# Optimization experiments

Measured on AMD Instinct MI355X. Metric: run time of the kernel, lower is better.

## Reference

```python
import jax, jax.numpy as jnp
import numpy as np

B, T, C, H = 4, 2048, 768, 12
D = C // H  # head dim = 64

def setup_inputs() -> dict:
    key = jax.random.key(0)
    k1, k2, k3, k4, k5 = jax.random.split(key, 5)
    s = 0.02
    x = jax.random.normal(k1, (B, T, C), dtype=jnp.float32)
    w_qkv = jax.random.normal(k2, (3 * C, C), dtype=jnp.float32) * s  # torch Linear weight [out,in]
    b_qkv = jax.random.normal(k3, (3 * C,), dtype=jnp.float32) * s
    w_proj = jax.random.normal(k4, (C, C), dtype=jnp.float32) * s
    b_proj = jax.random.normal(k5, (C,), dtype=jnp.float32) * s
    return {"x": x, "w_qkv": w_qkv, "b_qkv": b_qkv, "w_proj": w_proj, "b_proj": b_proj}

def reference(x, w_qkv, b_qkv, w_proj, b_proj):
    Bx, Tx, Cx = x.shape
    # qkv projection: torch Linear y = x @ W.T + b
    qkv = x @ w_qkv.T + b_qkv                      # [B,T,3C]
    qkv = qkv.reshape(Bx, Tx, 3, H, D)
    q, k, v = qkv[:, :, 0], qkv[:, :, 1], qkv[:, :, 2]  # each [B,T,H,D]
    scale = 1.0 / jnp.sqrt(jnp.float32(D))
    scores = jnp.einsum('bqhd,bkhd->bhqk', q, k) * scale  # [B,H,T,T]
    causal = jnp.tril(jnp.ones((Tx, Tx), dtype=bool))
    scores = jnp.where(causal[None, None], scores, -jnp.inf)
    attn = jax.nn.softmax(scores, axis=-1)
    out = jnp.einsum('bhqk,bkhd->bqhd', attn, v).reshape(Bx, Tx, Cx)
    return out @ w_proj.T + b_proj
```

## Files before the change

kernel.cpp:

```cpp
#include <hip/hip_runtime.h>
#include <hip/hip_bf16.h>
#include <cstdint>
#include <cstddef>

typedef __bf16 bf16_t;
typedef __bf16 bf16x8 __attribute__((ext_vector_type(8)));
typedef __bf16 bf16x4 __attribute__((ext_vector_type(4)));
typedef float f32x4 __attribute__((ext_vector_type(4)));
typedef float f32x16 __attribute__((ext_vector_type(16)));

constexpr int B_ = 4, T_ = 2048, C_ = 768, H_ = 12, D_ = 64;
constexpr size_t QKV_ELEMS = (size_t)B_ * H_ * T_ * D_;

__device__ __forceinline__ void gload16(const bf16_t* g, bf16_t* l) {
    __builtin_amdgcn_global_load_lds(
        (const __attribute__((address_space(1))) unsigned int*)g,
        (__attribute__((address_space(3))) unsigned int*)l, 16, 0, 0);
}

__global__ __launch_bounds__(256)
void conv_bf16(const float* __restrict__ a, bf16_t* __restrict__ oa, int na8,
               const float* __restrict__ b, bf16_t* __restrict__ ob, int nb8)
{
    int i = blockIdx.x * 256 + threadIdx.x;
    if (i >= na8 + nb8) return;
    const float* src; bf16_t* dst; int idx;
    if (i < na8) { src = a; dst = oa; idx = i; }
    else         { src = b; dst = ob; idx = i - na8; }
    const float4* p = reinterpret_cast<const float4*>(src + (size_t)idx * 8);
    float4 f0 = p[0], f1 = p[1];
    bf16x8 t;
    t[0]=(bf16_t)f0.x; t[1]=(bf16_t)f0.y; t[2]=(bf16_t)f0.z; t[3]=(bf16_t)f0.w;
    t[4]=(bf16_t)f1.x; t[5]=(bf16_t)f1.y; t[6]=(bf16_t)f1.z; t[7]=(bf16_t)f1.w;
    *reinterpret_cast<bf16x8*>(dst + (size_t)idx * 8) = t;
}

__global__ __launch_bounds__(256, 3)
void qkv_gemm(const bf16_t* __restrict__ xb, const bf16_t* __restrict__ wb,
              const float* __restrict__ bias,
              bf16_t* __restrict__ q, bf16_t* __restrict__ k, bf16_t* __restrict__ v)
{
    __shared__ alignas(16) bf16_t As[128 * 64];
    __shared__ alignas(16) bf16_t Bs[128 * 64];
    const int tid  = threadIdx.x;
    const int lane = tid & 63;
    const int w    = tid >> 6;
    const int wm = w >> 1, wn = w & 1;
    const int bm = blockIdx.x & 63;
    const int bn = blockIdx.x >> 6;
    const int m0 = bm * 128, n0 = bn * 128;
    const int lcol = lane & 15, lgrp = lane >> 4;
    const int srow = lane >> 3;
    const int scol = ((lane & 7) ^ srow) * 8;

    const bf16_t* ag = xb + (size_t)(m0 + w * 32 + srow) * C_ + scol;
    const bf16_t* bg = wb + (size_t)(n0 + w * 32 + srow) * C_ + scol;
    bf16_t* al = &As[(w * 32) * 64];
    bf16_t* bl = &Bs[(w * 32) * 64];

    f32x4 acc[4][4] = {};

    for (int kt = 0; kt < C_; kt += 64) {
        __syncthreads();
        #pragma unroll
        for (int p = 0; p < 4; ++p) {
            gload16(ag + (size_t)(p * 8) * C_ + kt, al + p * 8 * 64);
            gload16(bg + (size_t)(p * 8) * C_ + kt, bl + p * 8 * 64);
        }
        __syncthreads();
        #pragma unroll
        for (int kk = 0; kk < 2; ++kk) {
            bf16x8 af[4], bfr[4];
            #pragma unroll
            for (int i = 0; i < 4; ++i) {
                const int R = wm * 64 + i * 16 + lcol;
                af[i] = *reinterpret_cast<const bf16x8*>(&As[R * 64 + (((kk*4 + lgrp) ^ (R & 7)) << 3)]);
            }
            #pragma unroll
            for (int j = 0; j < 4; ++j) {
                const int R = wn * 64 + j * 16 + lcol;
                bfr[j] = *reinterpret_cast<const bf16x8*>(&Bs[R * 64 + (((kk*4 + lgrp) ^ (R & 7)) << 3)]);
            }
            #pragma unroll
            for (int i = 0; i < 4; ++i)
                #pragma unroll
                for (int j = 0; j < 4; ++j)
                    acc[i][j] = __builtin_amdgcn_mfma_f32_16x16x32_bf16(af[i], bfr[j], acc[i][j], 0, 0, 0);
        }
    }

    #pragma unroll
    for (int j = 0; j < 4; ++j) {
        const int n = n0 + wn * 64 + j * 16 + lcol;
        const float bv = bias[n];
        const int s = n / C_, rem = n % C_;
        const int h = rem >> 6, d = rem & 63;
        bf16_t* dst = (s == 0) ? q : (s == 1) ? k : v;
        #pragma unroll
        for (int i = 0; i < 4; ++i) {
            #pragma unroll
            for (int r = 0; r < 4; ++r) {
                const int m = m0 + wm * 64 + i * 16 + lgrp * 4 + r;
                const int b = m >> 11, t = m & (T_ - 1);
                dst[(((size_t)(b * H_ + h)) * T_ + t) * D_ + d] = (bf16_t)(acc[i][j][r] + bv);
            }
        }
    }
}

__global__ __launch_bounds__(128, 3)
void attn_fwd(const bf16_t* __restrict__ qg, const bf16_t* __restrict__ kg,
              const bf16_t* __restrict__ vg, bf16_t* __restrict__ og)
{
    __shared__ alignas(16) bf16_t Ks[64 * 64];
    __shared__ alignas(16) bf16_t Vt[64 * 64];

    const int tid  = threadIdx.x;
    const int lane = tid & 63;
    const int w    = tid >> 6;
    const int l31  = lane & 31;
    const int hi   = lane >> 5;
    const int qi   = blockIdx.x / 48;
    const int bh   = blockIdx.x % 48;
    const int qt   = 31 - qi;
    const int q0   = qt * 64;
    const int qw   = q0 + w * 32;
    const size_t base = (size_t)bh * T_ * D_;
    const int qrow = qw + l31;

    const float SCL = 0.125f * 1.44269504f;
    bf16x8 bq[4];
    #pragma unroll
    for (int kt = 0; kt < 4; ++kt) {
        bf16x8 t = *reinterpret_cast<const bf16x8*>(qg + base + (size_t)qrow * D_ + kt*16 + hi*8);
        #pragma unroll
        for (int e = 0; e < 8; ++e) t[e] = (bf16_t)((float)t[e] * SCL);
        bq[kt] = t;
    }

    f32x16 ot0 = {};
    f32x16 ot1 = {};
    float m = -1e30f, rowl = 0.0f;

    const int skey = tid >> 3;
    const int sgr  = tid & 7;
    const bf16_t* srcK = kg + base + (size_t)skey * D_ + sgr * 8;
    const bf16_t* srcV = vg + base + (size_t)(2 * skey) * D_ + sgr * 8;

    union U8 { bf16x8 v; uint32_t u[4]; };
    U8 kr[4], vr[2][2];

    #pragma unroll
    for (int p = 0; p < 4; ++p)
        kr[p].v = *reinterpret_cast<const bf16x8*>(srcK + (size_t)(p * 16) * D_);
    #pragma unroll
    for (int p = 0; p < 2; ++p) {
        vr[p][0].v = *reinterpret_cast<const bf16x8*>(srcV + (size_t)(p * 32) * D_);
        vr[p][1].v = *reinterpret_cast<const bf16x8*>(srcV + (size_t)(p * 32 + 1) * D_);
    }

    union UP { uint32_t u[4]; bf16x8 v; };

    const int ntiles = qt + 1;
    for (int it = 0; it < ntiles; ++it) {
        __syncthreads();
        #pragma unroll
        for (int p = 0; p < 4; ++p) {
            const int key = p * 16 + skey;
            *reinterpret_cast<bf16x8*>(Ks + key * 64 + ((sgr ^ (key & 7)) << 3)) = kr[p].v;
        }
        #pragma unroll
        for (int p = 0; p < 2; ++p) {
            const int va = p * 16 + skey;
            #pragma unroll
            for (int j = 0; j < 8; ++j) {
                const int d = sgr * 8 + j;
                const int ss = ((va >> 2) ^ j ^ sgr) & 7;
                uint32_t wd = __builtin_amdgcn_perm(vr[p][1].u[j >> 1], vr[p][0].u[j >> 1],
                                                    (j & 1) ? 0x07060302u : 0x05040100u);
                *reinterpret_cast<uint32_t*>(Vt + d * 64 + ss * 8 + (va & 3) * 2) = wd;
            }
        }
        __syncthreads();
        if (it + 1 < ntiles) {
            const size_t soff = (size_t)(it + 1) * 64 * D_;
            #pragma unroll
            for (int p = 0; p < 4; ++p)
                kr[p].v = *reinterpret_cast<const bf16x8*>(srcK + soff + (size_t)(p * 16) * D_);
            #pragma unroll
            for (int p = 0; p < 2; ++p) {
                vr[p][0].v = *reinterpret_cast<const bf16x8*>(srcV + soff + (size_t)(p * 32) * D_);
                vr[p][1].v = *reinterpret_cast<const bf16x8*>(srcV + soff + (size_t)(p * 32 + 1) * D_);
            }
        }

        const int kv0 = it * 64;
        #pragma unroll
        for (int sk = 0; sk < 2; ++sk) {
            const int kvs = kv0 + sk * 32;
            if (sk == 1 && kvs > qw + 31) continue;

            f32x16 s = {};
            __builtin_amdgcn_s_setprio(1);
            #pragma unroll
            for (int kt = 0; kt < 4; ++kt) {
                const int keyl = sk * 32 + l31;
                const int slot = kt * 2 + hi;
                bf16x8 ka = *reinterpret_cast<const bf16x8*>(
                    Ks + keyl * 64 + ((slot ^ (keyl & 7)) << 3));
                s = __builtin_amdgcn_mfma_f32_32x32x16_bf16(ka, bq[kt], s, 0, 0, 0);
            }
            __builtin_amdgcn_s_setprio(0);
            if (kvs + 31 > qw) {
                #pragma unroll
                for (int r = 0; r < 16; ++r) {
                    const int key = kvs + (r & 3) + 8 * (r >> 2) + 4 * hi;
                    if (key > qrow) s[r] = -1e30f;
                }
            }
            float a0 = fmaxf(fmaxf(s[0],  s[1]),  s[2]);
            float a1 = fmaxf(fmaxf(s[3],  s[4]),  s[5]);
            float a2 = fmaxf(fmaxf(s[6],  s[7]),  s[8]);
            float a3 = fmaxf(fmaxf(s[9],  s[10]), s[11]);
            float a4 = fmaxf(fmaxf(s[12], s[13]), s[14]);
            float b0 = fmaxf(fmaxf(a0, a1), a2);
            float b1 = fmaxf(fmaxf(a3, a4), s[15]);
            float mt = fmaxf(b0, b1);
            mt = fmaxf(mt, __shfl_xor(mt, 32));
            if (!__all(mt <= m + 8.0f)) {
                const float mnew = fmaxf(m, mt);
                const float alpha = exp2f(m - mnew);
                #pragma unroll
                for (int r = 0; r < 16; ++r) { ot0[r] *= alpha; ot1[r] *= alpha; }
                rowl *= alpha;
                m = mnew;
            }
            #pragma unroll
            for (int r = 0; r < 16; ++r) s[r] = exp2f(s[r] - m);
            float t0 = (s[0]+s[1]) + (s[2]+s[3]);
            float t1 = (s[4]+s[5]) + (s[6]+s[7]);
            float t2 = (s[8]+s[9]) + (s[10]+s[11]);
            float t3 = (s[12]+s[13]) + (s[14]+s[15]);
            float rs = (t0 + t1) + (t2 + t3);
            rs += __shfl_xor(rs, 32);
            rowl += rs;

            uint32_t c0, c1, c2, c3, c4, c5, c6, c7;
            asm("v_cvt_pk_bf16_f32 %0, %1, %2" : "=v"(c0) : "v"(s[0]),  "v"(s[1]));
            asm("v_cvt_pk_bf16_f32 %0, %1, %2" : "=v"(c1) : "v"(s[2]),  "v"(s[3]));
            asm("v_cvt_pk_bf16_f32 %0, %1, %2" : "=v"(c2) : "v"(s[4]),  "v"(s[5]));
            asm("v_cvt_pk_bf16_f32 %0, %1, %2" : "=v"(c3) : "v"(s[6]),  "v"(s[7]));
            asm("v_cvt_pk_bf16_f32 %0, %1, %2" : "=v"(c4) : "v"(s[8]),  "v"(s[9]));
            asm("v_cvt_pk_bf16_f32 %0, %1, %2" : "=v"(c5) : "v"(s[10]), "v"(s[11]));
            asm("v_cvt_pk_bf16_f32 %0, %1, %2" : "=v"(c6) : "v"(s[12]), "v"(s[13]));
            asm("v_cvt_pk_bf16_f32 %0, %1, %2" : "=v"(c7) : "v"(s[14]), "v"(s[15]));
            asm("v_permlane32_swap_b32 %0, %1" : "+v"(c0), "+v"(c2));
            asm("v_permlane32_swap_b32 %0, %1" : "+v"(c1), "+v"(c3));
            asm("v_permlane32_swap_b32 %0, %1" : "+v"(c4), "+v"(c6));
            asm("v_permlane32_swap_b32 %0, %1" : "+v"(c5), "+v"(c7));
            UP pa0; pa0.u[0] = c0; pa0.u[1] = c1; pa0.u[2] = c2; pa0.u[3] = c3;
            UP pa1; pa1.u[0] = c4; pa1.u[1] = c5; pa1.u[2] = c6; pa1.u[3] = c7;

            __builtin_amdgcn_s_setprio(1);
            #pragma unroll
            for (int dblk = 0; dblk < 2; ++dblk) {
                const int d = dblk * 32 + l31;
                f32x16& o = dblk ? ot1 : ot0;
                #pragma unroll
                for (int ktile = 0; ktile < 2; ++ktile) {
                    const int kslot = sk * 4 + ktile * 2 + hi;
                    const int ss = kslot ^ (d & 7) ^ ((d >> 3) & 7);
                    bf16x8 va = *reinterpret_cast<const bf16x8*>(Vt + d * 64 + (ss << 3));
                    o = __builtin_amdgcn_mfma_f32_32x32x16_bf16(va, ktile ? pa1.v : pa0.v, o, 0, 0, 0);
                }
            }
            __builtin_amdgcn_s_setprio(0);
        }
    }

    const int b = bh / H_, h = bh % H_;
    const float inv = 1.0f / rowl;
    bf16_t* dst = &og[((size_t)b * T_ + qrow) * C_ + h * D_];
    #pragma unroll
    for (int dblk = 0; dblk < 2; ++dblk) {
        const f32x16& o = dblk ? ot1 : ot0;
        #pragma unroll
        for (int qd = 0; qd < 4; ++qd) {
            bf16x4 v4;
            #pragma unroll
            for (int r = 0; r < 4; ++r) v4[r] = (bf16_t)(o[qd * 4 + r] * inv);
            *reinterpret_cast<bf16x4*>(dst + dblk * 32 + qd * 8 + hi * 4) = v4;
        }
    }
}

__global__ __launch_bounds__(256, 3)
void proj_gemm(const bf16_t* __restrict__ ao, const bf16_t* __restrict__ wpb,
               const float* __restrict__ bias, float* __restrict__ out)
{
    __shared__ alignas(16) bf16_t As[128 * 64];
    __shared__ alignas(16) bf16_t Bs[128 * 64];
    const int tid  = threadIdx.x;
    const int lane = tid & 63;
    const int w    = tid >> 6;
    const int wm = w >> 1, wn = w & 1;
    const int bm = blockIdx.x & 63;
    const int bn = blockIdx.x >> 6;
    const int m0 = bm * 128, n0 = bn * 128;
    const int lcol = lane & 15, lgrp = lane >> 4;
    const int srow = lane >> 3;
    const int scol = ((lane & 7) ^ srow) * 8;

    const bf16_t* ag = ao  + (size_t)(m0 + w * 32 + srow) * C_ + scol;
    const bf16_t* bg = wpb + (size_t)(n0 + w * 32 + srow) * C_ + scol;
    bf16_t* al = &As[(w * 32) * 64];
    bf16_t* bl = &Bs[(w * 32) * 64];

    f32x4 acc[4][4] = {};

    for (int kt = 0; kt < C_; kt += 64) {
        __syncthreads();
        #pragma unroll
        for (int p = 0; p < 4; ++p) {
            gload16(ag + (size_t)(p * 8) * C_ + kt, al + p * 8 * 64);
            gload16(bg + (size_t)(p * 8) * C_ + kt, bl + p * 8 * 64);
        }
        __syncthreads();
        #pragma unroll
        for (int kk = 0; kk < 2; ++kk) {
            bf16x8 af[4], bfr[4];
            #pragma unroll
            for (int i = 0; i < 4; ++i) {
                const int R = wm * 64 + i * 16 + lcol;
                af[i] = *reinterpret_cast<const bf16x8*>(&As[R * 64 + (((kk*4 + lgrp) ^ (R & 7)) << 3)]);
            }
            #pragma unroll
            for (int j = 0; j < 4; ++j) {
                const int R = wn * 64 + j * 16 + lcol;
                bfr[j] = *reinterpret_cast<const bf16x8*>(&Bs[R * 64 + (((kk*4 + lgrp) ^ (R & 7)) << 3)]);
            }
            #pragma unroll
            for (int i = 0; i < 4; ++i)
                #pragma unroll
                for (int j = 0; j < 4; ++j)
                    acc[i][j] = __builtin_amdgcn_mfma_f32_16x16x32_bf16(af[i], bfr[j], acc[i][j], 0, 0, 0);
        }
    }

    #pragma unroll
    for (int j = 0; j < 4; ++j) {
        const int n = n0 + wn * 64 + j * 16 + lcol;
        const float bv = bias[n];
        #pragma unroll
        for (int i = 0; i < 4; ++i) {
            #pragma unroll
            for (int r = 0; r < 4; ++r) {
                const int m = m0 + wm * 64 + i * 16 + lgrp * 4 + r;
                out[(size_t)m * C_ + n] = acc[i][j][r] + bv;
            }
        }
    }
}

extern "C" void kernel_launch(void* const* d_in, const int* in_sizes, int n_in,
                              void* d_out, int out_size, void* d_ws, size_t ws_size,
                              hipStream_t stream)
{
    const float* x      = (const float*)d_in[0];
    const float* w_qkv  = (const float*)d_in[1];
    const float* b_qkv  = (const float*)d_in[2];
    const float* w_proj = (const float*)d_in[3];
    const float* b_proj = (const float*)d_in[4];
    float* out = (float*)d_out;

    bf16_t* ws = (bf16_t*)d_ws;
    bf16_t* q   = ws;
    bf16_t* k   = ws +     QKV_ELEMS;
    bf16_t* v   = ws + 2 * QKV_ELEMS;
    bf16_t* ao  = ws + 3 * QKV_ELEMS;
    bf16_t* xb  = ao;
    bf16_t* wqb = (bf16_t*)d_out;
    bf16_t* wpb = k;

    conv_bf16<<<dim3(3936), 256, 0, stream>>>(x, xb, 786432, w_qkv, wqb, 221184);
    qkv_gemm<<<dim3(64 * 18), 256, 0, stream>>>(xb, wqb, b_qkv, q, k, v);
    attn_fwd<<<dim3(32 * 48), 128, 0, stream>>>(q, k, v, ao);
    conv_bf16<<<dim3(288), 256, 0, stream>>>(w_proj, wpb, 73728, w_proj, wpb, 0);
    proj_gemm<<<dim3(64 * 6), 256, 0, stream>>>(ao, wpb, b_proj, out);
}
```

Baseline: 135.3 us.

## Split attention KV loop across two wave pairs and merge partial softmax

The attention block grows from 2 to 4 waves. Each pair of waves handles alternate 64-key tiles from a double-width LDS buffer, so the KV loop is split in two (split-K style). Partial outputs, max and sum are merged through LDS at the end with an online-softmax rescale. This aims to cut per-block serial loop length and raise parallelism. In exchange it drops the register prefetch of the next tile, doubles LDS use, and adds a final merge step through shared memory.

```diff
diff --git a/kernel.cpp b/kernel.cpp
--- a/kernel.cpp
+++ b/kernel.cpp
@@ -108,23 +108,27 @@
     }
 }
 
-__global__ __launch_bounds__(128, 3)
+__global__ __launch_bounds__(256, 3)
 void attn_fwd(const bf16_t* __restrict__ qg, const bf16_t* __restrict__ kg,
               const bf16_t* __restrict__ vg, bf16_t* __restrict__ og)
 {
-    __shared__ alignas(16) bf16_t Ks[64 * 64];
-    __shared__ alignas(16) bf16_t Vt[64 * 64];
+    __shared__ alignas(16) bf16_t lds[4 * 64 * 64];
+    bf16_t* Ks = lds;
+    bf16_t* Vt = lds + 2 * 64 * 64;
+    float*  scr = (float*)lds;
 
     const int tid  = threadIdx.x;
     const int lane = tid & 63;
     const int w    = tid >> 6;
+    const int wq   = w >> 1;
+    const int ws   = w & 1;
     const int l31  = lane & 31;
     const int hi   = lane >> 5;
     const int qi   = blockIdx.x / 48;
     const int bh   = blockIdx.x % 48;
     const int qt   = 31 - qi;
     const int q0   = qt * 64;
-    const int qw   = q0 + w * 32;
+    const int qw   = q0 + wq * 32;
     const size_t base = (size_t)bh * T_ * D_;
     const int qrow = qw + l31;
 
@@ -142,59 +146,55 @@
     f32x16 ot1 = {};
     float m = -1e30f, rowl = 0.0f;
 
-    const int skey = tid >> 3;
-    const int sgr  = tid & 7;
-    const bf16_t* srcK = kg + base + (size_t)skey * D_ + sgr * 8;
-    const bf16_t* srcV = vg + base + (size_t)(2 * skey) * D_ + sgr * 8;
-
+    const int sgr = tid & 7;
     union U8 { bf16x8 v; uint32_t u[4]; };
-    U8 kr[4], vr[2][2];
-
-    #pragma unroll
-    for (int p = 0; p < 4; ++p)
-        kr[p].v = *reinterpret_cast<const bf16x8*>(srcK + (size_t)(p * 16) * D_);
-    #pragma unroll
-    for (int p = 0; p < 2; ++p) {
-        vr[p][0].v = *reinterpret_cast<const bf16x8*>(srcV + (size_t)(p * 32) * D_);
-        vr[p][1].v = *reinterpret_cast<const bf16x8*>(srcV + (size_t)(p * 32 + 1) * D_);
-    }
-
     union UP { uint32_t u[4]; bf16x8 v; };
 
     const int ntiles = qt + 1;
-    for (int it = 0; it < ntiles; ++it) {
-        __syncthreads();
-        #pragma unroll
-        for (int p = 0; p < 4; ++p) {
-            const int key = p * 16 + skey;
-            *reinterpret_cast<bf16x8*>(Ks + key * 64 + ((sgr ^ (key & 7)) << 3)) = kr[p].v;
-        }
-        #pragma unroll
-        for (int p = 0; p < 2; ++p) {
-            const int va = p * 16 + skey;
-            #pragma unroll
-            for (int j = 0; j < 8; ++j) {
-                const int d = sgr * 8 + j;
-                const int ss = ((va >> 2) ^ j ^ sgr) & 7;
-                uint32_t wd = __builtin_amdgcn_perm(vr[p][1].u[j >> 1], vr[p][0].u[j >> 1],
-                                                    (j & 1) ? 0x07060302u : 0x05040100u);
-                *reinterpret_cast<uint32_t*>(Vt + d * 64 + ss * 8 + (va & 3) * 2) = wd;
-            }
-        }
-        __syncthreads();
-        if (it + 1 < ntiles) {
-            const size_t soff = (size_t)(it + 1) * 64 * D_;
-            #pragma unroll
-            for (int p = 0; p < 4; ++p)
-                kr[p].v = *reinterpret_cast<const bf16x8*>(srcK + soff + (size_t)(p * 16) * D_);
-            #pragma unroll
-            for (int p = 0; p < 2; ++p) {
-                vr[p][0].v = *reinterpret_cast<const bf16x8*>(srcV + soff + (size_t)(p * 32) * D_);
-                vr[p][1].v = *reinterpret_cast<const bf16x8*>(srcV + soff + (size_t)(p * 32 + 1) * D_);
-            }
-        }
-
-        const int kv0 = it * 64;
+    const int np = (ntiles + 1) >> 1;
+
+    for (int p = 0; p < np; ++p) {
+        __syncthreads();
+        #pragma unroll
+        for (int par = 0; par < 2; ++par) {
+            const int t = 2 * p + par;
+            if (t >= ntiles) break;
+            const size_t toff = (size_t)t * 64 * D_;
+            #pragma unroll
+            for (int pp = 0; pp < 2; ++pp) {
+                const int g = pp * 256 + tid;
+                const int key = g >> 3, slot = g & 7;
+                bf16x8 kv = *reinterpret_cast<const bf16x8*>(
+                    kg + base + toff + (size_t)key * D_ + slot * 8);
+                *reinterpret_cast<bf16x8*>(
+                    Ks + par * 4096 + key * 64 + ((slot ^ (key & 7)) << 3)) = kv;
+            }
+            {
+                const int va = tid >> 3;
+                U8 v0, v1;
+                v0.v = *reinterpret_cast<const bf16x8*>(
+                    vg + base + toff + (size_t)(2 * va) * D_ + sgr * 8);
+                v1.v = *reinterpret_cast<const bf16x8*>(
+                    vg + base + toff + (size_t)(2 * va + 1) * D_ + sgr * 8);
+                #pragma unroll
+                for (int j = 0; j < 8; ++j) {
+                    const int d = sgr * 8 + j;
+                    const int ss = ((va >> 2) ^ j ^ sgr) & 7;
+                    uint32_t wd = __builtin_amdgcn_perm(v1.u[j >> 1], v0.u[j >> 1],
+                                                        (j & 1) ? 0x07060302u : 0x05040100u);
+                    *reinterpret_cast<uint32_t*>(
+                        Vt + par * 4096 + d * 64 + ss * 8 + (va & 3) * 2) = wd;
+                }
+            }
+        }
+        __syncthreads();
+
+        const int t = 2 * p + ws;
+        if (t >= ntiles) continue;
+        const bf16_t* Kb = Ks + ws * 4096;
+        const bf16_t* Vb = Vt + ws * 4096;
+        const int kv0 = t * 64;
+
         #pragma unroll
         for (int sk = 0; sk < 2; ++sk) {
             const int kvs = kv0 + sk * 32;
@@ -207,7 +207,7 @@
                 const int keyl = sk * 32 + l31;
                 const int slot = kt * 2 + hi;
                 bf16x8 ka = *reinterpret_cast<const bf16x8*>(
-                    Ks + keyl * 64 + ((slot ^ (keyl & 7)) << 3));
+                    Kb + keyl * 64 + ((slot ^ (keyl & 7)) << 3));
                 s = __builtin_amdgcn_mfma_f32_32x32x16_bf16(ka, bq[kt], s, 0, 0, 0);
             }
             __builtin_amdgcn_s_setprio(0);
@@ -270,7 +270,7 @@
                 for (int ktile = 0; ktile < 2; ++ktile) {
                     const int kslot = sk * 4 + ktile * 2 + hi;
                     const int ss = kslot ^ (d & 7) ^ ((d >> 3) & 7);
-                    bf16x8 va = *reinterpret_cast<const bf16x8*>(Vt + d * 64 + (ss << 3));
+                    bf16x8 va = *reinterpret_cast<const bf16x8*>(Vb + d * 64 + (ss << 3));
                     o = __builtin_amdgcn_mfma_f32_32x32x16_bf16(va, ktile ? pa1.v : pa0.v, o, 0, 0, 0);
                 }
             }
@@ -278,18 +278,36 @@
         }
     }
 
-    const int b = bh / H_, h = bh % H_;
-    const float inv = 1.0f / rowl;
-    bf16_t* dst = &og[((size_t)b * T_ + qrow) * C_ + h * D_];
-    #pragma unroll
-    for (int dblk = 0; dblk < 2; ++dblk) {
-        const f32x16& o = dblk ? ot1 : ot0;
-        #pragma unroll
-        for (int qd = 0; qd < 4; ++qd) {
-            bf16x4 v4;
-            #pragma unroll
-            for (int r = 0; r < 4; ++r) v4[r] = (bf16_t)(o[qd * 4 + r] * inv);
-            *reinterpret_cast<bf16x4*>(dst + dblk * 32 + qd * 8 + hi * 4) = v4;
+    __syncthreads();
+    if (ws == 1) {
+        float* s = scr + (wq * 64 + lane) * 35;
+        #pragma unroll
+        for (int r = 0; r < 16; ++r) { s[r] = ot0[r]; s[16 + r] = ot1[r]; }
+        s[32] = m; s[33] = rowl;
+    }
+    __syncthreads();
+    if (ws == 0) {
+        const float* s = scr + (wq * 64 + lane) * 35;
+        const float m1 = s[32], l1 = s[33];
+        const float mn = fmaxf(m, m1);
+        const float f0 = exp2f(m - mn);
+        const float f1 = exp2f(m1 - mn);
+        const float linv = 1.0f / (rowl * f0 + l1 * f1);
+        const int b = bh / H_, h = bh % H_;
+        bf16_t* dst = &og[((size_t)b * T_ + qrow) * C_ + h * D_];
+        #pragma unroll
+        for (int dblk = 0; dblk < 2; ++dblk) {
+            const f32x16& o = dblk ? ot1 : ot0;
+            #pragma unroll
+            for (int qd = 0; qd < 4; ++qd) {
+                bf16x4 v4;
+                #pragma unroll
+                for (int r = 0; r < 4; ++r) {
+                    const float ov = o[qd * 4 + r] * f0 + s[dblk * 16 + qd * 4 + r] * f1;
+                    v4[r] = (bf16_t)(ov * linv);
+                }
+                *reinterpret_cast<bf16x4*>(dst + dblk * 32 + qd * 8 + hi * 4) = v4;
+            }
         }
     }
 }
@@ -384,7 +402,7 @@
 
     conv_bf16<<<dim3(3936), 256, 0, stream>>>(x, xb, 786432, w_qkv, wqb, 221184);
     qkv_gemm<<<dim3(64 * 18), 256, 0, stream>>>(xb, wqb, b_qkv, q, k, v);
-    attn_fwd<<<dim3(32 * 48), 128, 0, stream>>>(q, k, v, ao);
+    attn_fwd<<<dim3(32 * 48), 256, 0, stream>>>(q, k, v, ao);
     conv_bf16<<<dim3(288), 256, 0, stream>>>(w_proj, wpb, 73728, w_proj, wpb, 0);
     proj_gemm<<<dim3(64 * 6), 256, 0, stream>>>(ao, wpb, b_proj, out);
 }
```

Result: faster. 120.8 us (-10.7%).
